# Kernel optimization log

Hardware: AMD Instinct MI355X
Metric: run time of the kernel (lower is better)

Reference implementation:

```python
import math
import jax, jax.numpy as jnp
import numpy as np

H = 1024
N2 = 32  # N // 2 complex state modes
DT_MIN, DT_MAX = 0.001, 0.1
L_DEFAULT = 4096


def setup_inputs() -> dict:
    key = jax.random.key(0)
    kC, kCa, kE, kdt = jax.random.split(key, 4)
    # Complex params stored as (..., 2) real pairs, matching torch.view_as_real.
    C_r = jax.random.normal(kC, (H, N2, 2), dtype=jnp.float32)
    C_aux_r = jax.random.normal(kCa, (H, N2, 2), dtype=jnp.float32)
    E_r = jax.random.normal(kE, (H, N2, 2), dtype=jnp.float32)
    # log_dt ~ U[log(dt_min), log(dt_max)]
    u = jax.random.uniform(kdt, (H,), dtype=jnp.float32)
    log_dt = u * (math.log(DT_MAX) - math.log(DT_MIN)) + math.log(DT_MIN)
    # A initialization: real part log(0.5), imag part pi * n (S4D-Lin)
    log_A_real = jnp.full((H, N2), math.log(0.5), dtype=jnp.float32)
    A_imag = math.pi * jnp.broadcast_to(jnp.arange(N2, dtype=jnp.float32), (H, N2))
    return {
        "C_r": C_r, "C_aux_r": C_aux_r, "E_r": E_r,
        "log_dt": log_dt, "log_A_real": log_A_real, "A_imag": A_imag,
        "L": L_DEFAULT,
    }


def _to_c(x):
    return jax.lax.complex(x[..., 0], x[..., 1])


def reference(C_r, C_aux_r, E_r, log_dt, log_A_real, A_imag, L):
    C = _to_c(C_r)          # (H, N2) complex
    C_aux = _to_c(C_aux_r)  # (H, N2)
    E = _to_c(E_r)          # (H, N2)

    A = jax.lax.complex(-jnp.exp(log_A_real), A_imag)  # (H, N2)
    dt = jnp.exp(log_dt)                               # (H,)
    dtA = A * dt[:, None]                              # (H, N2)

    # Vandermonde: exp(dtA * l) for l in [0, L) -> (H, N2, L) complex (the big intermediate)
    expK = jnp.exp(dtA[:, :, None] * jnp.arange(L, dtype=jnp.float32))

    scale = (jnp.exp(dtA) - 1.0) / A   # ZOH-like discretization factor
    C_main = C * scale
    C_aux_d = C_aux * scale
    E_main = E * C_main
    E_aux = E * C_aux_d

    Ku = 2.0 * jnp.einsum('hn,hnl->hl', C_main, expK).real
    Kx = 2.0 * jnp.einsum('hn,hnl->hl', E_main, expK).real
    Ku_aux = 2.0 * jnp.einsum('hn,hnl->hl', C_aux_d, expK).real
    Kx_aux = 2.0 * jnp.einsum('hn,hnl->hl', E_aux, expK).real
    return (Ku, Kx, Ku_aux, Kx_aux)
```

## Files before the change

kernel.cpp:

```cpp
#include <hip/hip_runtime.h>
#include <hip/hip_bf16.h>
#include <math.h>


typedef float    f32x2 __attribute__((ext_vector_type(2)));
typedef float    f32x4 __attribute__((ext_vector_type(4)));
typedef _Float16 half8 __attribute__((ext_vector_type(8)));

#define NMODES 32

__global__ __launch_bounds__(256, 4) void s4d_mfma_kernel(
    const float* __restrict__ C_r,
    const float* __restrict__ Ca_r,
    const float* __restrict__ E_r,
    const float* __restrict__ log_dt,
    const float* __restrict__ log_A_real,
    const float* __restrict__ A_imag,
    float* __restrict__ out,
    int H, int N2, int L)
{
    const int h    = blockIdx.x;
    const int tid  = threadIdx.x;
    const int w    = tid >> 6;
    const int lane = tid & 63;
    const int l15  = lane & 15;
    const int lgrp = lane >> 4;

    __shared__ _Float16 Bt_hi[64][72];
    __shared__ _Float16 Bt_lo[64][72];
    __shared__ f32x4 s_anc[NMODES];
    __shared__ f32x2 s_r  [NMODES];
    __shared__ f32x2 s_G  [NMODES];
    __shared__ f32x2 s_coef[4][NMODES];

    if (tid < N2) {
        const int n = tid;
        const double ldt  = (double)log_dt[h];
        const double dtd  = exp(ldt);
        const float  dtf  = (float)dtd;
        const float  aref = -__expf(log_A_real[h * N2 + n]);
        const float  aimf = A_imag[h * N2 + n];
        const float  dre  = aref * dtf;
        const double dim  = (double)aimf * dtd;
        const double dimrev = dim * 0.15915494309189535;

        float hi = (float)dimrev;
        hi = __uint_as_float(__float_as_uint(hi) & 0xFFFFF000u);
        const float lo = (float)(dimrev - (double)hi);

        const float trev = (float)(dimrev - rint(dimrev));
        const float sn = __builtin_amdgcn_sinf(trev);
        const float cs = __builtin_amdgcn_cosf(trev);
        const float er = __expf(dre);
        const float Ere = er * cs, Eim = er * sn;

        const double d1024 = dimrev * 1024.0;
        const float  g_t   = (float)(d1024 - rint(d1024));
        const float  g_er  = __expf(dre * 1024.0f);
        f32x2 G;
        G.x = g_er * __builtin_amdgcn_cosf(g_t);
        G.y = g_er * __builtin_amdgcn_sinf(g_t);

        const float sh  = __builtin_amdgcn_sinf(0.5f * trev);
        const float cs1 = -2.f * sh * sh;
        const float nr  = expm1f(dre) + er * cs1;
        const float ni  = er * sn;
        const float den = aref * aref + aimf * aimf;
        const float scr = (nr * aref + ni * aimf) / den;
        const float sci = (ni * aref - nr * aimf) / den;

        const float cr  = C_r [(h * N2 + n) * 2 + 0];
        const float ci  = C_r [(h * N2 + n) * 2 + 1];
        const float ar  = Ca_r[(h * N2 + n) * 2 + 0];
        const float ai  = Ca_r[(h * N2 + n) * 2 + 1];
        const float exr = E_r [(h * N2 + n) * 2 + 0];
        const float exi = E_r [(h * N2 + n) * 2 + 1];
        const float cmr = cr * scr - ci * sci;
        const float cmi = cr * sci + ci * scr;
        const float car = ar * scr - ai * sci;
        const float cai = ar * sci + ai * scr;
        const float emr = exr * cmr - exi * cmi;
        const float emi = exr * cmi + exi * cmr;
        const float ear = exr * car - exi * cai;
        const float eai = exr * cai + exi * car;

        f32x2 c;
        c.x = 2.f*cmr; c.y = 2.f*cmi; s_coef[0][n] = c;
        c.x = 2.f*emr; c.y = 2.f*emi; s_coef[1][n] = c;
        c.x = 2.f*car; c.y = 2.f*cai; s_coef[2][n] = c;
        c.x = 2.f*ear; c.y = 2.f*eai; s_coef[3][n] = c;

        f32x4 a;
        a.x = dre; a.y = hi; a.z = lo; a.w = 0.f;
        s_anc[n] = a;
        f32x2 rv; rv.x = Ere; rv.y = Eim;
        s_r[n] = rv;
        s_G[n] = G;
    }
    __syncthreads();

    {
        const int n   = tid >> 3;
        const int l2b = (tid & 7) * 8;
        const f32x4 an = s_anc[n];
        const f32x2 rv = s_r[n];
        const float l2f = (float)l2b;
        float t = an.y * l2f;  t -= rintf(t);
        t = fmaf(an.z, l2f, t); t -= rintf(t);
        const float er = __expf(an.x * l2f);
        float qr = er * __builtin_amdgcn_cosf(t);
        float qi = er * __builtin_amdgcn_sinf(t);
#pragma unroll
        for (int j = 0; j < 8; ++j) {
            const int l2 = l2b + j;
            const _Float16 qrh = (_Float16)qr;
            Bt_hi[l2][n] = qrh;
            Bt_lo[l2][n] = (_Float16)(qr - (float)qrh);
            const float mi = -qi;
            const _Float16 mih = (_Float16)mi;
            Bt_hi[l2][n + 32] = mih;
            Bt_lo[l2][n + 32] = (_Float16)(mi - (float)mih);
            if (j < 7) {
                const float nqr = fmaf(qr, rv.x, -(qi * rv.y));
                qi = fmaf(qr, rv.y, qi * rv.x);
                qr = nqr;
            }
        }
    }

    half8 ahi[4][2], alo[4][2];
    {
        const int nb = lgrp * 8;
        const float rowf = 64.f * (float)l15;
#pragma unroll
        for (int j = 0; j < 8; ++j) {
            const int n = nb + j;
            const f32x4 an = s_anc[n];
            const f32x2 c  = s_coef[w][n];
            const f32x2 G  = s_G[n];
            float t = an.y * rowf;  t -= rintf(t);
            t = fmaf(an.z, rowf, t); t -= rintf(t);
            const float er = __expf(an.x * rowf);
            const float pr = er * __builtin_amdgcn_cosf(t);
            const float pi = er * __builtin_amdgcn_sinf(t);
            float zr = c.x * pr - c.y * pi;
            float zi = c.x * pi + c.y * pr;
#pragma unroll
            for (int tm = 0; tm < 4; ++tm) {
                const _Float16 zrh = (_Float16)zr;
                const _Float16 zih = (_Float16)zi;
                ahi[tm][0][j] = zrh;
                alo[tm][0][j] = (_Float16)(zr - (float)zrh);
                ahi[tm][1][j] = zih;
                alo[tm][1][j] = (_Float16)(zi - (float)zih);
                if (tm < 3) {
                    const float nzr = fmaf(zr, G.x, -(zi * G.y));
                    zi = fmaf(zr, G.y, zi * G.x);
                    zr = nzr;
                }
            }
        }
    }
    __syncthreads();

    const size_t HL = (size_t)H * (size_t)L;
    float* obase = out + (size_t)w * HL + (size_t)h * (size_t)L;

#pragma unroll
    for (int tn = 0; tn < 4; ++tn) {
        const int brow = 16 * tn + l15;
        const half8 bh0 = *(const half8*)&Bt_hi[brow][ 8 * lgrp];
        const half8 bh1 = *(const half8*)&Bt_hi[brow][32 + 8 * lgrp];
        const half8 bl0 = *(const half8*)&Bt_lo[brow][ 8 * lgrp];
        const half8 bl1 = *(const half8*)&Bt_lo[brow][32 + 8 * lgrp];
#pragma unroll
        for (int tm = 0; tm < 4; ++tm) {
            f32x4 acc = {0.f, 0.f, 0.f, 0.f};
            acc = __builtin_amdgcn_mfma_f32_16x16x32_f16(ahi[tm][0], bh0, acc, 0, 0, 0);
            acc = __builtin_amdgcn_mfma_f32_16x16x32_f16(ahi[tm][1], bh1, acc, 0, 0, 0);
            acc = __builtin_amdgcn_mfma_f32_16x16x32_f16(ahi[tm][0], bl0, acc, 0, 0, 0);
            acc = __builtin_amdgcn_mfma_f32_16x16x32_f16(ahi[tm][1], bl1, acc, 0, 0, 0);
            acc = __builtin_amdgcn_mfma_f32_16x16x32_f16(alo[tm][0], bh0, acc, 0, 0, 0);
            acc = __builtin_amdgcn_mfma_f32_16x16x32_f16(alo[tm][1], bh1, acc, 0, 0, 0);
#pragma unroll
            for (int i = 0; i < 4; ++i) {
                const int r = 16 * tm + 4 * lgrp + i;
                obase[64 * r + 16 * tn + l15] = acc[i];
            }
        }
    }
}

extern "C" void kernel_launch(void* const* d_in, const int* in_sizes, int n_in,
                              void* d_out, int out_size, void* d_ws, size_t ws_size,
                              hipStream_t stream) {
    const float* C_r        = (const float*)d_in[0];
    const float* Ca_r       = (const float*)d_in[1];
    const float* E_r        = (const float*)d_in[2];
    const float* log_dt     = (const float*)d_in[3];
    const float* log_A_real = (const float*)d_in[4];
    const float* A_imag     = (const float*)d_in[5];
    float* out = (float*)d_out;

    const int H  = in_sizes[3];
    const int N2 = in_sizes[4] / H;
    const int L  = out_size / (4 * H);

    dim3 grid(H);
    dim3 block(256);
    s4d_mfma_kernel<<<grid, block, 0, stream>>>(
        C_r, Ca_r, E_r, log_dt, log_A_real, A_imag, out, H, N2, L);
}
```

Baseline: 91.04 us.

## Evaluate B-tile powers directly, vectorise LDS writes, shorten A recurrence, nontemporal stores

New measurement: 94.84 us. 4.2% more time.

```diff
diff --git a/kernel.cpp b/kernel.cpp
--- a/kernel.cpp
+++ b/kernel.cpp
@@ -29,7 +29,6 @@
     __shared__ _Float16 Bt_hi[64][72];
     __shared__ _Float16 Bt_lo[64][72];
     __shared__ f32x4 s_anc[NMODES];
-    __shared__ f32x2 s_r  [NMODES];
     __shared__ f32x2 s_G  [NMODES];
     __shared__ f32x2 s_coef[4][NMODES];
 
@@ -50,9 +49,7 @@
 
         const float trev = (float)(dimrev - rint(dimrev));
         const float sn = __builtin_amdgcn_sinf(trev);
-        const float cs = __builtin_amdgcn_cosf(trev);
         const float er = __expf(dre);
-        const float Ere = er * cs, Eim = er * sn;
 
         const double d1024 = dimrev * 1024.0;
         const float  g_t   = (float)(d1024 - rint(d1024));
@@ -93,72 +90,84 @@
         f32x4 a;
         a.x = dre; a.y = hi; a.z = lo; a.w = 0.f;
         s_anc[n] = a;
-        f32x2 rv; rv.x = Ere; rv.y = Eim;
-        s_r[n] = rv;
         s_G[n] = G;
     }
     __syncthreads();
 
     {
-        const int n   = tid >> 3;
-        const int l2b = (tid & 7) * 8;
-        const f32x4 an = s_anc[n];
-        const f32x2 rv = s_r[n];
-        const float l2f = (float)l2b;
-        float t = an.y * l2f;  t -= rintf(t);
-        t = fmaf(an.z, l2f, t); t -= rintf(t);
-        const float er = __expf(an.x * l2f);
-        float qr = er * __builtin_amdgcn_cosf(t);
-        float qi = er * __builtin_amdgcn_sinf(t);
+        const int l2 = tid >> 2;
+        const int nb = (tid & 3) * 8;
+        const float l2f = (float)l2;
+        half8 qh, ql, mh, ml;
 #pragma unroll
         for (int j = 0; j < 8; ++j) {
-            const int l2 = l2b + j;
+            const f32x4 an = s_anc[nb + j];
+            float t = an.y * l2f;  t -= rintf(t);
+            t = fmaf(an.z, l2f, t); t -= rintf(t);
+            const float er = __expf(an.x * l2f);
+            const float qr = er * __builtin_amdgcn_cosf(t);
+            const float qi = er * __builtin_amdgcn_sinf(t);
             const _Float16 qrh = (_Float16)qr;
-            Bt_hi[l2][n] = qrh;
-            Bt_lo[l2][n] = (_Float16)(qr - (float)qrh);
+            qh[j] = qrh;
+            ql[j] = (_Float16)(qr - (float)qrh);
             const float mi = -qi;
             const _Float16 mih = (_Float16)mi;
-            Bt_hi[l2][n + 32] = mih;
-            Bt_lo[l2][n + 32] = (_Float16)(mi - (float)mih);
-            if (j < 7) {
-                const float nqr = fmaf(qr, rv.x, -(qi * rv.y));
-                qi = fmaf(qr, rv.y, qi * rv.x);
-                qr = nqr;
-            }
+            mh[j] = mih;
+            ml[j] = (_Float16)(mi - (float)mih);
         }
+        *(half8*)&Bt_hi[l2][nb]      = qh;
+        *(half8*)&Bt_hi[l2][nb + 32] = mh;
+        *(half8*)&Bt_lo[l2][nb]      = ql;
+        *(half8*)&Bt_lo[l2][nb + 32] = ml;
     }
 
     half8 ahi[4][2], alo[4][2];
     {
-        const int nb = lgrp * 8;
-        const float rowf = 64.f * (float)l15;
+        const int nbw = lgrp * 8;
+        const float row0 = 64.f * (float)l15;
+        const float row2 = 2048.f + row0;
 #pragma unroll
         for (int j = 0; j < 8; ++j) {
-            const int n = nb + j;
+            const int n = nbw + j;
             const f32x4 an = s_anc[n];
             const f32x2 c  = s_coef[w][n];
             const f32x2 G  = s_G[n];
-            float t = an.y * rowf;  t -= rintf(t);
-            t = fmaf(an.z, rowf, t); t -= rintf(t);
-            const float er = __expf(an.x * rowf);
-            const float pr = er * __builtin_amdgcn_cosf(t);
-            const float pi = er * __builtin_amdgcn_sinf(t);
-            float zr = c.x * pr - c.y * pi;
-            float zi = c.x * pi + c.y * pr;
-#pragma unroll
-            for (int tm = 0; tm < 4; ++tm) {
-                const _Float16 zrh = (_Float16)zr;
-                const _Float16 zih = (_Float16)zi;
-                ahi[tm][0][j] = zrh;
-                alo[tm][0][j] = (_Float16)(zr - (float)zrh);
-                ahi[tm][1][j] = zih;
-                alo[tm][1][j] = (_Float16)(zi - (float)zih);
-                if (tm < 3) {
-                    const float nzr = fmaf(zr, G.x, -(zi * G.y));
-                    zi = fmaf(zr, G.y, zi * G.x);
-                    zr = nzr;
-                }
-            }
+
+            float t0 = an.y * row0;  t0 -= rintf(t0);
+            t0 = fmaf(an.z, row0, t0); t0 -= rintf(t0);
+            const float e0 = __expf(an.x * row0);
+            const float p0r = e0 * __builtin_amdgcn_cosf(t0);
+            const float p0i = e0 * __builtin_amdgcn_sinf(t0);
+
+            float t2 = an.y * row2;  t2 -= rintf(t2);
+            t2 = fmaf(an.z, row2, t2); t2 -= rintf(t2);
+            const float e2 = __expf(an.x * row2);
+            const float p2r = e2 * __builtin_amdgcn_cosf(t2);
+            const float p2i = e2 * __builtin_amdgcn_sinf(t2);
+
+            float zr = c.x * p0r - c.y * p0i;
+            float zi = c.x * p0i + c.y * p0r;
+            _Float16 zrh = (_Float16)zr, zih = (_Float16)zi;
+            ahi[0][0][j] = zrh; alo[0][0][j] = (_Float16)(zr - (float)zrh);
+            ahi[0][1][j] = zih; alo[0][1][j] = (_Float16)(zi - (float)zih);
+
+            float yr = fmaf(zr, G.x, -(zi * G.y));
+            float yi = fmaf(zr, G.y,  (zi * G.x));
+            zrh = (_Float16)yr; zih = (_Float16)yi;
+            ahi[1][0][j] = zrh; alo[1][0][j] = (_Float16)(yr - (float)zrh);
+            ahi[1][1][j] = zih; alo[1][1][j] = (_Float16)(yi - (float)zih);
+
+            zr = c.x * p2r - c.y * p2i;
+            zi = c.x * p2i + c.y * p2r;
+            zrh = (_Float16)zr; zih = (_Float16)zi;
+            ahi[2][0][j] = zrh; alo[2][0][j] = (_Float16)(zr - (float)zrh);
+            ahi[2][1][j] = zih; alo[2][1][j] = (_Float16)(zi - (float)zih);
+
+            yr = fmaf(zr, G.x, -(zi * G.y));
+            yi = fmaf(zr, G.y,  (zi * G.x));
+            zrh = (_Float16)yr; zih = (_Float16)yi;
+            ahi[3][0][j] = zrh; alo[3][0][j] = (_Float16)(yr - (float)zrh);
+            ahi[3][1][j] = zih; alo[3][1][j] = (_Float16)(yi - (float)zih);
         }
     }
     __syncthreads();
@@ -185,7 +194,7 @@
 #pragma unroll
             for (int i = 0; i < 4; ++i) {
                 const int r = 16 * tm + 4 * lgrp + i;
-                obase[64 * r + 16 * tn + l15] = acc[i];
+                __builtin_nontemporal_store(acc[i], &obase[64 * r + 16 * tn + l15]);
             }
         }
     }
```
